# Optimization experiments

Measured on AMD Instinct MI355X. Metric: run time of the kernel, lower is better.

The kernel has to match this reference:

```python
import jax, jax.numpy as jnp
import numpy as np

EMBED_DIM = 128
HIDDEN_DIM = 512
NUM_LAYERS = 2
LATENT_DIM = 128
VOCAB = 2048
BATCH = 4096
NEG = -1.0e9  # matches torch masked fill value -1e9
TEMPERATURE = 1.0  # generate() skips the divide when temperature == 1.0


def _gru_cell(x, h, w_ih, w_hh, b_ih, b_hh):
    # PyTorch GRU cell, gate order (r, z, n)
    gi = x @ w_ih.T + b_ih          # [B, 3H]
    gh = h @ w_hh.T + b_hh          # [B, 3H]
    i_r, i_z, i_n = jnp.split(gi, 3, axis=-1)
    h_r, h_z, h_n = jnp.split(gh, 3, axis=-1)
    r = jax.nn.sigmoid(i_r + h_r)
    u = jax.nn.sigmoid(i_z + h_z)
    n = jnp.tanh(i_n + r * h_n)
    return (1.0 - u) * n + u * h


def setup_inputs() -> dict:
    key = jax.random.key(0)
    ks = jax.random.split(key, 16)

    def unif(k, shape, fan):
        bound = 1.0 / np.sqrt(fan)
        return jax.random.uniform(k, shape, jnp.float32, -bound, bound)

    embed = jax.random.normal(ks[0], (VOCAB, EMBED_DIM), jnp.float32)
    embed = embed.at[0].set(0.0)  # padding_idx = 0

    return dict(
        z=jax.random.normal(ks[1], (BATCH, LATENT_DIM), jnp.float32),
        embed=embed,
        w_lh=unif(ks[2], (NUM_LAYERS * HIDDEN_DIM, LATENT_DIM), LATENT_DIM),
        b_lh=unif(ks[3], (NUM_LAYERS * HIDDEN_DIM,), LATENT_DIM),
        w_ih0=unif(ks[4], (3 * HIDDEN_DIM, EMBED_DIM), HIDDEN_DIM),
        w_hh0=unif(ks[5], (3 * HIDDEN_DIM, HIDDEN_DIM), HIDDEN_DIM),
        b_ih0=unif(ks[6], (3 * HIDDEN_DIM,), HIDDEN_DIM),
        b_hh0=unif(ks[7], (3 * HIDDEN_DIM,), HIDDEN_DIM),
        w_ih1=unif(ks[8], (3 * HIDDEN_DIM, HIDDEN_DIM), HIDDEN_DIM),
        w_hh1=unif(ks[9], (3 * HIDDEN_DIM, HIDDEN_DIM), HIDDEN_DIM),
        b_ih1=unif(ks[10], (3 * HIDDEN_DIM,), HIDDEN_DIM),
        b_hh1=unif(ks[11], (3 * HIDDEN_DIM,), HIDDEN_DIM),
        w_out=unif(ks[12], (VOCAB, HIDDEN_DIM), HIDDEN_DIM),
        b_out=unif(ks[13], (VOCAB,), HIDDEN_DIM),
        bos_idx=1, eos_idx=2, pad_idx=0,
        max_len=64, top_k=40, min_generation_length=20,
    )


def reference(z, embed, w_lh, b_lh, w_ih0, w_hh0, b_ih0, b_hh0,
              w_ih1, w_hh1, b_ih1, b_hh1, w_out, b_out,
              bos_idx, eos_idx, pad_idx, max_len, top_k, min_generation_length):
    B = z.shape[0]
    V = w_out.shape[0]
    H = w_hh0.shape[1]
    eff_min = max(0, min(int(min_generation_length), max(0, max_len - 2)))

    # latent -> initial hidden state [L, B, H]
    h = jnp.tanh(z @ w_lh.T + b_lh).reshape(B, NUM_LAYERS, H).transpose(1, 0, 2)
    rows = jnp.arange(B)[:, None]

    def step(carry, t):
        h, cur, finished, key = carry
        key, sk = jax.random.split(key)
        x = embed[cur]                                   # [B, E]
        h0 = _gru_cell(x, h[0], w_ih0, w_hh0, b_ih0, b_hh0)
        h1 = _gru_cell(h0, h[1], w_ih1, w_hh1, b_ih1, b_hh1)
        logits = h1 @ w_out.T + b_out                    # [B, V]
        logits = logits.at[:, bos_idx].set(NEG).at[:, pad_idx].set(NEG)
        # block EOS until min_generation_length real tokens emitted
        logits = jnp.where((t - 1) < eff_min, logits.at[:, eos_idx].set(NEG), logits)
        if TEMPERATURE != 1.0:
            logits = logits / max(TEMPERATURE, 1e-6)
        if 0 < top_k < V:
            tv, ti = jax.lax.top_k(logits, top_k)
            logits = jnp.full_like(logits, NEG).at[rows, ti].set(tv)
        # multinomial over softmax(logits) == categorical on logits
        nxt = jax.random.categorical(sk, logits).astype(jnp.int32)
        nxt = jnp.where(finished, pad_idx, nxt)
        finished = finished | (nxt == eos_idx)
        return (jnp.stack([h0, h1]), nxt, finished, key), nxt

    init = (h,
            jnp.full((B,), bos_idx, jnp.int32),
            jnp.zeros((B,), dtype=bool),
            jax.random.key(1))
    _, toks = jax.lax.scan(step, init, jnp.arange(1, max_len))  # toks: [max_len-1, B]
    return jnp.concatenate(
        [jnp.full((B, 1), bos_idx, jnp.int32), toks.T.astype(jnp.int32)], axis=1)
```

## Files before the change

kernel.cpp:

```cpp
#include <hip/hip_runtime.h>
#include <cstdint>
#include <cstddef>

#ifndef PARTITIONABLE
#define PARTITIONABLE 1
#endif

namespace {
constexpr int kBatch  = 4096;
constexpr int kEmb    = 128;
constexpr int kHid    = 512;
constexpr int kVoc    = 2048;
constexpr int kMaxLen = 64;
constexpr int kTopK   = 40;
constexpr int kBos = 1, kEos = 2, kPad = 0;
constexpr int kEffMin = 20;
constexpr float kNeg  = -1.0e9f;
constexpr float kTiny = 1.17549435082228751e-38f;
}

typedef __bf16 bf16x8 __attribute__((ext_vector_type(8)));
typedef float  f32x4  __attribute__((ext_vector_type(4)));

__host__ __device__ inline void tf2x32(uint32_t k0, uint32_t k1,
                                       uint32_t x0, uint32_t x1,
                                       uint32_t& o0, uint32_t& o1) {
  uint32_t ks0 = k0, ks1 = k1, ks2 = k0 ^ k1 ^ 0x1BD11BDAu;
  x0 += ks0; x1 += ks1;
#define TFR(r) { x0 += x1; x1 = (x1 << (r)) | (x1 >> (32 - (r))); x1 ^= x0; }
  TFR(13) TFR(15) TFR(26) TFR(6)   x0 += ks1; x1 += ks2 + 1u;
  TFR(17) TFR(29) TFR(16) TFR(24)  x0 += ks2; x1 += ks0 + 2u;
  TFR(13) TFR(15) TFR(26) TFR(6)   x0 += ks0; x1 += ks1 + 3u;
  TFR(17) TFR(29) TFR(16) TFR(24)  x0 += ks1; x1 += ks2 + 4u;
  TFR(13) TFR(15) TFR(26) TFR(6)   x0 += ks2; x1 += ks0 + 5u;
#undef TFR
  o0 = x0; o1 = x1;
}

__device__ __forceinline__ float xla_tanh(float x) {
  float ax = fabsf(x);
  float xc = fminf(fmaxf(x, -9.0f), 9.0f);
  float x2 = __fmul_rn(xc, xc);
  float num = -2.76076847742355e-16f;
  num = __fadd_rn(__fmul_rn(x2, num), 2.00018790482477e-13f);
  num = __fadd_rn(__fmul_rn(x2, num), -8.60467152213735e-11f);
  num = __fadd_rn(__fmul_rn(x2, num), 5.12229709037114e-08f);
  num = __fadd_rn(__fmul_rn(x2, num), 1.48572235717979e-05f);
  num = __fadd_rn(__fmul_rn(x2, num), 6.37261928875436e-04f);
  num = __fadd_rn(__fmul_rn(x2, num), 4.89352455891786e-03f);
  num = __fmul_rn(xc, num);
  float den = 1.19825839466702e-06f;
  den = __fadd_rn(__fmul_rn(x2, den), 1.18534705686654e-04f);
  den = __fadd_rn(__fmul_rn(x2, den), 2.26843463243900e-03f);
  den = __fadd_rn(__fmul_rn(x2, den), 4.89352518554385e-03f);
  return (ax < 4.0e-04f) ? x : __fdiv_rn(num, den);
}

__device__ __forceinline__ float xla_sigmoid(float x) {
  return __fdiv_rn(1.0f, __fadd_rn(1.0f, expf(-x)));
}

__device__ __forceinline__ void gl_lds16(const void* g, void* l) {
  __builtin_amdgcn_global_load_lds(
      (const __attribute__((address_space(1))) void*)g,
      (__attribute__((address_space(3))) void*)l, 16, 0, 0);
}

__device__ __forceinline__ void split3(float a, __bf16& a0, __bf16& a1, __bf16& a2) {
  a0 = (__bf16)a;
  float r1 = __fsub_rn(a, (float)a0);
  a1 = (__bf16)r1;
  float r2 = __fsub_rn(r1, (float)a1);
  a2 = (__bf16)r2;
}

__device__ __forceinline__ float gru_h(float gir, float giz, float gin,
                                       float ghr, float ghz, float ghn,
                                       float hold) {
  float r = xla_sigmoid(__fadd_rn(gir, ghr));
  float u = xla_sigmoid(__fadd_rn(giz, ghz));
  float n = xla_tanh(__fadd_rn(gin, __fmul_rn(r, ghn)));
  float t1 = __fmul_rn(__fsub_rn(1.0f, u), n);
  float t2 = __fmul_rn(u, hold);
  return __fadd_rn(t1, t2);
}

#define MFMA9(c, A0_, A1_, A2_, B0_, B1_, B2_) do {                          \
    c = __builtin_amdgcn_mfma_f32_16x16x32_bf16(A2_, B2_, c, 0, 0, 0);       \
    c = __builtin_amdgcn_mfma_f32_16x16x32_bf16(A2_, B1_, c, 0, 0, 0);       \
    c = __builtin_amdgcn_mfma_f32_16x16x32_bf16(A1_, B2_, c, 0, 0, 0);       \
    c = __builtin_amdgcn_mfma_f32_16x16x32_bf16(A2_, B0_, c, 0, 0, 0);       \
    c = __builtin_amdgcn_mfma_f32_16x16x32_bf16(A1_, B1_, c, 0, 0, 0);       \
    c = __builtin_amdgcn_mfma_f32_16x16x32_bf16(A0_, B2_, c, 0, 0, 0);       \
    c = __builtin_amdgcn_mfma_f32_16x16x32_bf16(A1_, B0_, c, 0, 0, 0);       \
    c = __builtin_amdgcn_mfma_f32_16x16x32_bf16(A0_, B1_, c, 0, 0, 0);       \
    c = __builtin_amdgcn_mfma_f32_16x16x32_bf16(A0_, B0_, c, 0, 0, 0);       \
  } while (0)

template <int ACT>
__global__ __launch_bounds__(256) void gemm2(
    const float* __restrict__ A0, const float* __restrict__ B0,
    const float* __restrict__ bias0, float* __restrict__ C0,
    const float* __restrict__ A1, const float* __restrict__ B1,
    const float* __restrict__ bias1, float* __restrict__ C1,
    int lda, int ldb, int ldc, int K) {
  __shared__ __attribute__((aligned(16))) float As[2][128 * 16];
  __shared__ __attribute__((aligned(16))) float Bs[2][16 * 128];

  const float* A    = blockIdx.z ? A1 : A0;
  const float* Bt   = blockIdx.z ? B1 : B0;
  const float* bias = blockIdx.z ? bias1 : bias0;
  float*       C    = blockIdx.z ? C1 : C0;

  const int tid = threadIdx.x;
  const int w = tid >> 6, l = tid & 63;
  const int bm = blockIdx.y * 128;
  const int bn = blockIdx.x * 128;
  const int tx = tid & 15, ty = tid >> 4;
  const int t3 = ty & 3;

  const int arow  = w * 16 + (l >> 2);
  const int agran = (l & 3) ^ ((l >> 2) & 3);
  const float* pA = A + (size_t)(bm + arow) * lda + agran * 4;
  const int bk = w * 2 + (l >> 5);
  const int bnc = (l & 31) * 4;
  const float* pB = Bt + (size_t)bk * ldb + bn + bnc;

  float acc[8][8];
#pragma unroll
  for (int i = 0; i < 8; ++i)
#pragma unroll
    for (int j = 0; j < 8; ++j) acc[i][j] = 0.0f;

  const int nt = K >> 4;
  gl_lds16(pA,            &As[0][w * 256]);
  gl_lds16(pA + 64 * lda, &As[0][(4 + w) * 256]);
  gl_lds16(pB,            &Bs[0][w * 256]);
  gl_lds16(pB + (size_t)8 * ldb, &Bs[0][(4 + w) * 256]);
  __syncthreads();

  for (int t = 0; t < nt; ++t) {
    const int cur = t & 1;
    if (t + 1 < nt) {
      const float* qA = pA + (t + 1) * 16;
      const float* qB = pB + (size_t)(t + 1) * 16 * ldb;
      gl_lds16(qA,            &As[cur ^ 1][w * 256]);
      gl_lds16(qA + 64 * lda, &As[cur ^ 1][(4 + w) * 256]);
      gl_lds16(qB,            &Bs[cur ^ 1][w * 256]);
      gl_lds16(qB + (size_t)8 * ldb, &Bs[cur ^ 1][(4 + w) * 256]);
    }
    const float* as = As[cur];
    const float* bs = Bs[cur];
#pragma unroll
    for (int g = 0; g < 4; ++g) {
      float4 bv0[4], bv1[4];
#pragma unroll
      for (int q = 0; q < 4; ++q) {
        bv0[q] = *(const float4*)&bs[(g * 4 + q) * 128 + tx * 4];
        bv1[q] = *(const float4*)&bs[(g * 4 + q) * 128 + 64 + tx * 4];
      }
#pragma unroll
      for (int ii = 0; ii < 8; ++ii) {
        float4 a = *(const float4*)&as[(ty + 16 * ii) * 16 + ((g ^ t3) * 4)];
        float ak[4] = {a.x, a.y, a.z, a.w};
#pragma unroll
        for (int q = 0; q < 4; ++q) {
          const float av_ = ak[q];
          const float4 b0 = bv0[q], b1 = bv1[q];
          acc[ii][0] += av_ * b0.x; acc[ii][1] += av_ * b0.y;
          acc[ii][2] += av_ * b0.z; acc[ii][3] += av_ * b0.w;
          acc[ii][4] += av_ * b1.x; acc[ii][5] += av_ * b1.y;
          acc[ii][6] += av_ * b1.z; acc[ii][7] += av_ * b1.w;
        }
      }
    }
    __syncthreads();
  }

  const int c0 = bn + tx * 4, c1 = bn + 64 + tx * 4;
  const float4 bs0 = *(const float4*)&bias[c0];
  const float4 bs1 = *(const float4*)&bias[c1];
#pragma unroll
  for (int ii = 0; ii < 8; ++ii) {
    const int r = bm + ty + 16 * ii;
    float4 o0, o1;
    o0.x = acc[ii][0] + bs0.x; o0.y = acc[ii][1] + bs0.y;
    o0.z = acc[ii][2] + bs0.z; o0.w = acc[ii][3] + bs0.w;
    o1.x = acc[ii][4] + bs1.x; o1.y = acc[ii][5] + bs1.y;
    o1.z = acc[ii][6] + bs1.z; o1.w = acc[ii][7] + bs1.w;
    if (ACT == 1) {
      o0.x = xla_tanh(o0.x); o0.y = xla_tanh(o0.y);
      o0.z = xla_tanh(o0.z); o0.w = xla_tanh(o0.w);
      o1.x = xla_tanh(o1.x); o1.y = xla_tanh(o1.y);
      o1.z = xla_tanh(o1.z); o1.w = xla_tanh(o1.w);
    }
    *(float4*)(C + (size_t)r * ldc + c0) = o0;
    *(float4*)(C + (size_t)r * ldc + c1) = o1;
  }
}

struct GemmArgs {
  const __bf16 *a0, *a1, *a2;
  const __bf16 *b0, *b1, *b2;
  const float* bias;
  float* c;
};

__global__ __launch_bounds__(256, 3) void gemm_mx3(
    GemmArgs g0, GemmArgs g1, int N) {
  __shared__ __attribute__((aligned(16))) __bf16 lds[6 * 4096];

  const GemmArgs g = blockIdx.z ? g1 : g0;
  const int tid = threadIdx.x;
  const int nwg = gridDim.x * gridDim.y;
  const int lin = blockIdx.y * gridDim.x + blockIdx.x;
  const int swz = (lin & 7) * (nwg >> 3) + (lin >> 3);
  const int bm = (swz / gridDim.x) * 128;
  const int bn = (swz % gridDim.x) * 128;
  const int lane = tid & 63;
  const int w  = tid >> 6;
  const int wm = w & 1;
  const int wn = w >> 1;
  const int l15 = lane & 15;
  const int kge = (lane >> 4) * 8;

  const int srow = tid >> 2;
  const int sge  = (tid & 3) * 8;
  const __bf16* tp[6];
  tp[0] = g.a0 + (size_t)(bm + srow) * 512 + sge;
  tp[1] = g.a1 + (size_t)(bm + srow) * 512 + sge;
  tp[2] = g.a2 + (size_t)(bm + srow) * 512 + sge;
  tp[3] = g.b0 + (size_t)(bn + srow) * 512 + sge;
  tp[4] = g.b1 + (size_t)(bn + srow) * 512 + sge;
  tp[5] = g.b2 + (size_t)(bn + srow) * 512 + sge;

  int aoff[4], boff[4];
#pragma unroll
  for (int i = 0; i < 4; ++i) {
    aoff[i] = (wm * 64 + i * 16 + l15) * 32 + kge;
    boff[i] = (wn * 64 + i * 16 + l15) * 32 + kge;
  }

  f32x4 acc[4][4] = {};

  for (int s = 0; s < 16; ++s) {
    const int k0 = s * 32;
#pragma unroll
    for (int p = 0; p < 6; ++p) {
      gl_lds16(tp[p] + k0,                    &lds[p * 4096 + w * 512]);
      gl_lds16(tp[p] + (size_t)64 * 512 + k0, &lds[p * 4096 + 2048 + w * 512]);
    }
    __syncthreads();

    bf16x8 Af[3][4];
#pragma unroll
    for (int mi = 0; mi < 4; ++mi) {
      Af[0][mi] = *(const bf16x8*)&lds[0 * 4096 + aoff[mi]];
      Af[1][mi] = *(const bf16x8*)&lds[1 * 4096 + aoff[mi]];
      Af[2][mi] = *(const bf16x8*)&lds[2 * 4096 + aoff[mi]];
    }
#pragma unroll
    for (int nj = 0; nj < 4; ++nj) {
      bf16x8 B0 = *(const bf16x8*)&lds[3 * 4096 + boff[nj]];
      bf16x8 B1 = *(const bf16x8*)&lds[4 * 4096 + boff[nj]];
      bf16x8 B2 = *(const bf16x8*)&lds[5 * 4096 + boff[nj]];
#pragma unroll
      for (int mi = 0; mi < 4; ++mi) {
        f32x4 c = acc[mi][nj];
        MFMA9(c, Af[0][mi], Af[1][mi], Af[2][mi], B0, B1, B2);
        acc[mi][nj] = c;
      }
    }
    __syncthreads();
  }

#pragma unroll
  for (int mi = 0; mi < 4; ++mi) {
    const int row0 = bm + wm * 64 + mi * 16 + (lane >> 4) * 4;
#pragma unroll
    for (int nj = 0; nj < 4; ++nj) {
      const int col = bn + wn * 64 + nj * 16 + l15;
      const float bv = g.bias[col];
      f32x4 v = acc[mi][nj];
#pragma unroll
      for (int r = 0; r < 4; ++r)
        g.c[(size_t)(row0 + r) * N + col] = v[r] + bv;
    }
  }
}

__global__ __launch_bounds__(256, 2) void gemm_gru0(
    const __bf16* __restrict__ a0, const __bf16* __restrict__ a1,
    const __bf16* __restrict__ a2,
    const __bf16* __restrict__ wb0, const __bf16* __restrict__ wb1,
    const __bf16* __restrict__ wb2,
    const float* __restrict__ bias, const float* __restrict__ Eih0,
    const int* __restrict__ curTok,
    __bf16* __restrict__ q0, __bf16* __restrict__ q1,
    __bf16* __restrict__ q2) {
  __shared__ __attribute__((aligned(16))) __bf16 As[3][4096];
  __shared__ __attribute__((aligned(16))) __bf16 Bs[9][1024];

  const int tid = threadIdx.x;
  const int nwg = gridDim.x * gridDim.y;
  const int lin = blockIdx.y * gridDim.x + blockIdx.x;
  const int swz = (lin & 7) * (nwg >> 3) + (lin >> 3);
  const int bm = (swz / gridDim.x) * 128;
  const int bn = (swz % gridDim.x) * 32;
  const int lane = tid & 63;
  const int w  = tid >> 6;
  const int wm = w & 1;
  const int wn = w >> 1;
  const int l15 = lane & 15;
  const int kge = (lane >> 4) * 8;

  const int srow = tid >> 2;
  const int sge  = (tid & 3) * 8;
  const __bf16* tpA[3];
  tpA[0] = a0 + (size_t)(bm + srow) * 512 + sge;
  tpA[1] = a1 + (size_t)(bm + srow) * 512 + sge;
  tpA[2] = a2 + (size_t)(bm + srow) * 512 + sge;

  const int bcol = lane >> 2;
  const int bge  = (lane & 3) * 8;

  int aoff[4];
#pragma unroll
  for (int i = 0; i < 4; ++i)
    aoff[i] = (wm * 64 + i * 16 + l15) * 32 + kge;
  const int boff = (wn * 16 + l15) * 32 + kge;

  f32x4 acc[3][4] = {};

  for (int s = 0; s < 16; ++s) {
    const int k0 = s * 32;
#pragma unroll
    for (int p = 0; p < 3; ++p) {
      gl_lds16(tpA[p] + k0,                    &As[p][w * 512]);
      gl_lds16(tpA[p] + (size_t)64 * 512 + k0, &As[p][2048 + w * 512]);
    }
    for (int qq = w; qq < 9; qq += 4) {
      const int gg = qq / 3, pp = qq - gg * 3;
      const __bf16* wp = (pp == 0) ? wb0 : (pp == 1) ? wb1 : wb2;
      const __bf16* src =
          wp + (size_t)(gg * 512 + bn + bcol) * 512 + bge + k0;
      gl_lds16(src,                     &Bs[qq][0]);
      gl_lds16(src + (size_t)16 * 512,  &Bs[qq][512]);
    }
    __syncthreads();

    bf16x8 Af[3][4];
#pragma unroll
    for (int mi = 0; mi < 4; ++mi) {
      Af[0][mi] = *(const bf16x8*)&As[0][aoff[mi]];
      Af[1][mi] = *(const bf16x8*)&As[1][aoff[mi]];
      Af[2][mi] = *(const bf16x8*)&As[2][aoff[mi]];
    }
#pragma unroll
    for (int gg = 0; gg < 3; ++gg) {
      bf16x8 B0 = *(const bf16x8*)&Bs[gg * 3 + 0][boff];
      bf16x8 B1 = *(const bf16x8*)&Bs[gg * 3 + 1][boff];
      bf16x8 B2 = *(const bf16x8*)&Bs[gg * 3 + 2][boff];
#pragma unroll
      for (int mi = 0; mi < 4; ++mi) {
        f32x4 c = acc[gg][mi];
        MFMA9(c, Af[0][mi], Af[1][mi], Af[2][mi], B0, B1, B2);
        acc[gg][mi] = c;
      }
    }
    __syncthreads();
  }

  const int col = bn + wn * 16 + l15;
  const float bvr = bias[col];
  const float bvz = bias[512 + col];
  const float bvn = bias[1024 + col];
#pragma unroll
  for (int mi = 0; mi < 4; ++mi) {
    const int row0 = bm + wm * 64 + mi * 16 + (lane >> 4) * 4;
#pragma unroll
    for (int rr = 0; rr < 4; ++rr) {
      const int row = row0 + rr;
      const int tok = curTok[row];
      const float* e = Eih0 + (size_t)tok * 1536;
      const size_t idx = (size_t)row * 512 + col;
      float hold = __fadd_rn(__fadd_rn((float)a0[idx], (float)a1[idx]),
                             (float)a2[idx]);
      float hnew = gru_h(e[col], e[512 + col], e[1024 + col],
                         acc[0][mi][rr] + bvr, acc[1][mi][rr] + bvz,
                         acc[2][mi][rr] + bvn, hold);
      __bf16 s0, s1, s2;
      split3(hnew, s0, s1, s2);
      q0[idx] = s0; q1[idx] = s1; q2[idx] = s2;
    }
  }
}

__global__ __launch_bounds__(256, 2) void gemm_gru1(
    const __bf16* __restrict__ x0, const __bf16* __restrict__ x1,
    const __bf16* __restrict__ x2,
    const __bf16* __restrict__ wi0, const __bf16* __restrict__ wi1,
    const __bf16* __restrict__ wi2,
    const __bf16* __restrict__ wh0, const __bf16* __restrict__ wh1,
    const __bf16* __restrict__ wh2,
    const float* __restrict__ bias_i, const float* __restrict__ bias_h,
    const __bf16* __restrict__ hi0, const __bf16* __restrict__ hi1,
    const __bf16* __restrict__ hi2,
    __bf16* __restrict__ ho0, __bf16* __restrict__ ho1,
    __bf16* __restrict__ ho2) {
  __shared__ __attribute__((aligned(16))) __bf16 As[6][2048];
  __shared__ __attribute__((aligned(16))) __bf16 Bs[18][1024];

  const int tid = threadIdx.x;
  const int nwg = gridDim.x * gridDim.y;
  const int lin = blockIdx.y * gridDim.x + blockIdx.x;
  const int swz = (lin & 7) * (nwg >> 3) + (lin >> 3);
  const int bm = (swz / gridDim.x) * 64;
  const int bn = (swz % gridDim.x) * 32;
  const int lane = tid & 63;
  const int w  = tid >> 6;
  const int wm = w & 1;
  const int wn = w >> 1;
  const int l15 = lane & 15;
  const int kge = (lane >> 4) * 8;

  const int srow = tid >> 2;
  const int sge  = (tid & 3) * 8;
  const __bf16* tpA[6];
  tpA[0] = x0 + (size_t)(bm + srow) * 512 + sge;
  tpA[1] = x1 + (size_t)(bm + srow) * 512 + sge;
  tpA[2] = x2 + (size_t)(bm + srow) * 512 + sge;
  tpA[3] = hi0 + (size_t)(bm + srow) * 512 + sge;
  tpA[4] = hi1 + (size_t)(bm + srow) * 512 + sge;
  tpA[5] = hi2 + (size_t)(bm + srow) * 512 + sge;

  const int bcol = lane >> 2;
  const int bge  = (lane & 3) * 8;

  int aoff[2];
#pragma unroll
  for (int i = 0; i < 2; ++i)
    aoff[i] = (wm * 32 + i * 16 + l15) * 32 + kge;
  const int boff = (wn * 16 + l15) * 32 + kge;

  f32x4 acci[3][2] = {};
  f32x4 acch[3][2] = {};

  const __bf16* wis[3] = {wi0, wi1, wi2};
  const __bf16* whs[3] = {wh0, wh1, wh2};

  for (int s = 0; s < 16; ++s) {
    const int k0 = s * 32;
#pragma unroll
    for (int p = 0; p < 6; ++p)
      gl_lds16(tpA[p] + k0, &As[p][w * 512]);
    for (int qq = w; qq < 18; qq += 4) {
      const int wset = qq / 9;
      const int gg = (qq - wset * 9) / 3, pp = qq - wset * 9 - gg * 3;
      const __bf16* wp = wset ? whs[pp] : wis[pp];
      const __bf16* src = wp + (size_t)(gg * 512 + bn + bcol) * 512 + bge + k0;
      gl_lds16(src,                    &Bs[qq][0]);
      gl_lds16(src + (size_t)16 * 512, &Bs[qq][512]);
    }
    __syncthreads();

    bf16x8 Xf[3][2], Hf[3][2];
#pragma unroll
    for (int mi = 0; mi < 2; ++mi) {
      Xf[0][mi] = *(const bf16x8*)&As[0][aoff[mi]];
      Xf[1][mi] = *(const bf16x8*)&As[1][aoff[mi]];
      Xf[2][mi] = *(const bf16x8*)&As[2][aoff[mi]];
      Hf[0][mi] = *(const bf16x8*)&As[3][aoff[mi]];
      Hf[1][mi] = *(const bf16x8*)&As[4][aoff[mi]];
      Hf[2][mi] = *(const bf16x8*)&As[5][aoff[mi]];
    }
#pragma unroll
    for (int gg = 0; gg < 3; ++gg) {
      bf16x8 Bi0 = *(const bf16x8*)&Bs[gg * 3 + 0][boff];
      bf16x8 Bi1 = *(const bf16x8*)&Bs[gg * 3 + 1][boff];
      bf16x8 Bi2 = *(const bf16x8*)&Bs[gg * 3 + 2][boff];
      bf16x8 Bh0 = *(const bf16x8*)&Bs[9 + gg * 3 + 0][boff];
      bf16x8 Bh1 = *(const bf16x8*)&Bs[9 + gg * 3 + 1][boff];
      bf16x8 Bh2 = *(const bf16x8*)&Bs[9 + gg * 3 + 2][boff];
#pragma unroll
      for (int mi = 0; mi < 2; ++mi) {
        f32x4 ci = acci[gg][mi];
        MFMA9(ci, Xf[0][mi], Xf[1][mi], Xf[2][mi], Bi0, Bi1, Bi2);
        acci[gg][mi] = ci;
        f32x4 ch = acch[gg][mi];
        MFMA9(ch, Hf[0][mi], Hf[1][mi], Hf[2][mi], Bh0, Bh1, Bh2);
        acch[gg][mi] = ch;
      }
    }
    __syncthreads();
  }

  const int col = bn + wn * 16 + l15;
  const float bir = bias_i[col];
  const float biz = bias_i[512 + col];
  const float bin = bias_i[1024 + col];
  const float bhr = bias_h[col];
  const float bhz = bias_h[512 + col];
  const float bhn = bias_h[1024 + col];
#pragma unroll
  for (int mi = 0; mi < 2; ++mi) {
    const int row0 = bm + wm * 32 + mi * 16 + (lane >> 4) * 4;
#pragma unroll
    for (int rr = 0; rr < 4; ++rr) {
      const int row = row0 + rr;
      const size_t idx = (size_t)row * 512 + col;
      float hold = __fadd_rn(__fadd_rn((float)hi0[idx], (float)hi1[idx]),
                             (float)hi2[idx]);
      float hnew = gru_h(acci[0][mi][rr] + bir, acci[1][mi][rr] + biz,
                         acci[2][mi][rr] + bin,
                         acch[0][mi][rr] + bhr, acch[1][mi][rr] + bhz,
                         acch[2][mi][rr] + bhn, hold);
      __bf16 s0, s1, s2;
      split3(hnew, s0, s1, s2);
      ho0[idx] = s0; ho1[idx] = s1; ho2[idx] = s2;
    }
  }
}

__global__ __launch_bounds__(256) void k_split(
    const float* __restrict__ in, __bf16* __restrict__ p0,
    __bf16* __restrict__ p1, __bf16* __restrict__ p2, int total) {
  int i = blockIdx.x * 256 + threadIdx.x;
  if (i >= total) return;
  __bf16 a0, a1, a2;
  split3(in[i], a0, a1, a2);
  p0[i] = a0; p1[i] = a1; p2[i] = a2;
}

__global__ __launch_bounds__(256) void k_transpose(
    const float* __restrict__ in, float* __restrict__ out, int R, int C) {
  __shared__ float tile[32][33];
  int c0 = blockIdx.x * 32, r0 = blockIdx.y * 32;
  int x = threadIdx.x, y0 = threadIdx.y;
  for (int i = y0; i < 32; i += 8) {
    int r = r0 + i, c = c0 + x;
    tile[i][x] = (r < R && c < C) ? in[(size_t)r * C + c] : 0.0f;
  }
  __syncthreads();
  for (int i = y0; i < 32; i += 8) {
    int orow = c0 + i, oc = r0 + x;
    if (orow < C && oc < R) out[(size_t)orow * R + oc] = tile[x][i];
  }
}

__global__ __launch_bounds__(256) void k_sample(
    const float* __restrict__ logits, int* __restrict__ cur,
    int* __restrict__ finished, int* __restrict__ outTok,
    int t, uint32_t sk0, uint32_t sk1) {
  const int row = blockIdx.x;
  const int tid = threadIdx.x;
  __shared__ float sl[kVoc];
  __shared__ uint32_t skeys[kVoc];
  __shared__ int   redi[4];
  __shared__ float redf[4];
  __shared__ int   redix[4];

  const float* lp = logits + (size_t)row * kVoc;
  for (int c = tid; c < kVoc; c += 256) {
    float v = lp[c];
    if (c == kBos || c == kPad) v = kNeg;
    if (c == kEos && t < 1 + kEffMin) v = kNeg;
    sl[c] = v;
    uint32_t u = __float_as_uint(v);
    skeys[c] = u ^ ((u >> 31) ? 0xFFFFFFFFu : 0x80000000u);
  }
  __syncthreads();

  uint32_t prefix = 0u;
  for (int b = 31; b >= 0; --b) {
    uint32_t trial = prefix | (1u << b);
    int cnt = 0;
    for (int c = tid; c < kVoc; c += 256) cnt += (skeys[c] >= trial) ? 1 : 0;
#pragma unroll
    for (int off = 32; off; off >>= 1) cnt += __shfl_down(cnt, off, 64);
    __syncthreads();
    if ((tid & 63) == 0) redi[tid >> 6] = cnt;
    __syncthreads();
    int total = redi[0] + redi[1] + redi[2] + redi[3];
    if (total >= kTopK) prefix = trial;
  }

  float best = -3.4e38f; int bidx = kVoc;
  for (int c = tid; c < kVoc; c += 256) {
    if (skeys[c] >= prefix) {
      uint32_t idx = (uint32_t)row * (uint32_t)kVoc + (uint32_t)c;
      uint32_t w1, w2, bits;
#if PARTITIONABLE
      tf2x32(sk0, sk1, 0u, idx, w1, w2);
      bits = w1 ^ w2;
#else
      const uint32_t HH = (uint32_t)((uint64_t)kBatch * kVoc / 2);
      if (idx < HH) { tf2x32(sk0, sk1, idx, idx + HH, w1, w2); bits = w1; }
      else          { tf2x32(sk0, sk1, idx - HH, idx, w1, w2); bits = w2; }
#endif
      uint32_t fb = (bits >> 9) | 0x3f800000u;
      float uf = __fsub_rn(__uint_as_float(fb), 1.0f);
      if (uf == 0.0f) uf = kTiny;
      float g = -logf(-logf(uf));
      float tot = __fadd_rn(g, sl[c]);
      if (tot > best || (tot == best && c < bidx)) { best = tot; bidx = c; }
    }
  }
#pragma unroll
  for (int off = 32; off; off >>= 1) {
    float ov = __shfl_down(best, off, 64);
    int   oi = __shfl_down(bidx, off, 64);
    if (ov > best || (ov == best && oi < bidx)) { best = ov; bidx = oi; }
  }
  if ((tid & 63) == 0) { redf[tid >> 6] = best; redix[tid >> 6] = bidx; }
  __syncthreads();
  if (tid == 0) {
    for (int w = 1; w < 4; ++w) {
      if (redf[w] > best || (redf[w] == best && redix[w] < bidx)) {
        best = redf[w]; bidx = redix[w];
      }
    }
    int fin = finished[row];
    int nxt = fin ? kPad : bidx;
    outTok[(size_t)row * kMaxLen + t] = nxt;
    cur[row] = nxt;
    finished[row] = fin | (nxt == kEos);
  }
}

__global__ __launch_bounds__(256) void k_init(int* cur, int* finished, int* outTok) {
  int i = blockIdx.x * 256 + threadIdx.x;
  if (i < kBatch) {
    cur[i] = kBos;
    finished[i] = 0;
    outTok[(size_t)i * kMaxLen] = kBos;
  }
}

extern "C" void kernel_launch(void* const* d_in, const int* in_sizes, int n_in,
                              void* d_out, int out_size, void* d_ws, size_t ws_size,
                              hipStream_t stream) {
  (void)in_sizes; (void)n_in; (void)out_size; (void)ws_size;
  const float* z      = (const float*)d_in[0];
  const float* embed  = (const float*)d_in[1];
  const float* w_lh   = (const float*)d_in[2];
  const float* b_lh   = (const float*)d_in[3];
  const float* w_ih0  = (const float*)d_in[4];
  const float* w_hh0  = (const float*)d_in[5];
  const float* b_ih0  = (const float*)d_in[6];
  const float* b_hh0  = (const float*)d_in[7];
  const float* w_ih1  = (const float*)d_in[8];
  const float* w_hh1  = (const float*)d_in[9];
  const float* b_ih1  = (const float*)d_in[10];
  const float* b_hh1  = (const float*)d_in[11];
  const float* w_out  = (const float*)d_in[12];
  const float* b_out  = (const float*)d_in[13];
  int* out = (int*)d_out;

  char* base = (char*)d_ws;
  int* curTok   = (int*)base;
  int* finished = curTok + kBatch;
  __bf16* q = (__bf16*)(base + 32768);
  __bf16* whh0[3]; __bf16* wih1[3]; __bf16* whh1[3]; __bf16* wout[3];
  for (int i = 0; i < 3; ++i) { whh0[i] = q; q += (size_t)1536 * 512; }
  for (int i = 0; i < 3; ++i) { wih1[i] = q; q += (size_t)1536 * 512; }
  for (int i = 0; i < 3; ++i) { whh1[i] = q; q += (size_t)1536 * 512; }
  for (int i = 0; i < 3; ++i) { wout[i] = q; q += (size_t)2048 * 512; }
  __bf16* hs0A[3]; __bf16* hs1A[3];
  for (int i = 0; i < 3; ++i) { hs0A[i] = q; q += (size_t)kBatch * kHid; }
  for (int i = 0; i < 3; ++i) { hs1A[i] = q; q += (size_t)kBatch * kHid; }
  float* f = (float*)q;
  float* Eih0 = f; f += (size_t)kVoc * 1536;
  float* ghA  = f; f += (size_t)kBatch * 1536;
  float* gi1  = f; f += (size_t)kBatch * 1536;
  float* logits = ghA;
  float* wt_ih0 = ghA;
  float* wt_lh  = ghA + (size_t)128 * 1536;
  float* h0tmp  = gi1;
  float* h1tmp  = gi1 + (size_t)kBatch * kHid;
  __bf16* hs0B[3];
  { __bf16* hb = (__bf16*)f;
    for (int i = 0; i < 3; ++i) { hs0B[i] = hb; hb += (size_t)kBatch * kHid; } }
  __bf16* hs1B[3];
  {
    __bf16* hb = (__bf16*)(gi1 + (size_t)kBatch * kHid);
    for (int i = 0; i < 3; ++i) { hs1B[i] = hb; hb += (size_t)kBatch * kHid; } }

  dim3 blk(256);
  dim3 tblk(32, 8);

  k_transpose<<<dim3(4, 48), tblk, 0, stream>>>(w_ih0, wt_ih0, 1536, 128);
  k_transpose<<<dim3(4, 32), tblk, 0, stream>>>(w_lh,  wt_lh,  1024, 128);
  k_split<<<dim3(1536 * 512 / 256), blk, 0, stream>>>(w_hh0, whh0[0], whh0[1], whh0[2], 1536 * 512);
  k_split<<<dim3(1536 * 512 / 256), blk, 0, stream>>>(w_ih1, wih1[0], wih1[1], wih1[2], 1536 * 512);
  k_split<<<dim3(1536 * 512 / 256), blk, 0, stream>>>(w_hh1, whh1[0], whh1[1], whh1[2], 1536 * 512);
  k_split<<<dim3(2048 * 512 / 256), blk, 0, stream>>>(w_out, wout[0], wout[1], wout[2], 2048 * 512);

  gemm2<0><<<dim3(12, 16, 1), blk, 0, stream>>>(
      embed, wt_ih0, b_ih0, Eih0, embed, wt_ih0, b_ih0, Eih0,
      kEmb, 1536, 1536, kEmb);
  gemm2<1><<<dim3(4, 32, 2), blk, 0, stream>>>(
      z, wt_lh,       b_lh,       h0tmp,
      z, wt_lh + 512, b_lh + 512, h1tmp,
      kEmb, 1024, kHid, kEmb);
  k_split<<<dim3(kBatch * kHid / 256), blk, 0, stream>>>(h0tmp, hs0A[0], hs0A[1], hs0A[2], kBatch * kHid);
  k_split<<<dim3(kBatch * kHid / 256), blk, 0, stream>>>(h1tmp, hs1A[0], hs1A[1], hs1A[2], kBatch * kHid);
  k_init<<<dim3((kBatch + 255) / 256), blk, 0, stream>>>(curTok, finished, out);

  uint32_t key0 = 0u, key1 = 1u;
  for (int t = 1; t < kMaxLen; ++t) {
    uint32_t nk0, nk1, s0, s1;
#if PARTITIONABLE
    tf2x32(key0, key1, 0u, 0u, nk0, nk1);
    tf2x32(key0, key1, 0u, 1u, s0, s1);
#else
    uint32_t a0, b0w, a1, b1w;
    tf2x32(key0, key1, 0u, 2u, a0, b0w);
    tf2x32(key0, key1, 1u, 3u, a1, b1w);
    nk0 = a0; nk1 = a1; s0 = b0w; s1 = b1w;
#endif
    __bf16** h0in  = (t & 1) ? hs0A : hs0B;
    __bf16** h0out = (t & 1) ? hs0B : hs0A;
    __bf16** h1in  = (t & 1) ? hs1A : hs1B;
    __bf16** h1out = (t & 1) ? hs1B : hs1A;

    gemm_gru0<<<dim3(16, 32), blk, 0, stream>>>(
        h0in[0], h0in[1], h0in[2], whh0[0], whh0[1], whh0[2],
        b_hh0, Eih0, curTok, h0out[0], h0out[1], h0out[2]);

    gemm_gru1<<<dim3(16, 64), blk, 0, stream>>>(
        h0out[0], h0out[1], h0out[2],
        wih1[0], wih1[1], wih1[2],
        whh1[0], whh1[1], whh1[2],
        b_ih1, b_hh1,
        h1in[0], h1in[1], h1in[2],
        h1out[0], h1out[1], h1out[2]);

    GemmArgs gla{h1out[0], h1out[1], h1out[2], wout[0], wout[1], wout[2], b_out, logits};
    gemm_mx3<<<dim3(16, 32, 1), blk, 0, stream>>>(gla, gla, 2048);
    k_sample<<<dim3(kBatch), blk, 0, stream>>>(logits, curTok, finished, out, t, s0, s1);

    key0 = nk0; key1 = nk1;
  }
}
```

Measured before the change: 19.81 ms.

## Enlarge GRU1 M-tile with phased X/H loads; radix-select top-k threshold

The layer-1 GRU GEMM now uses a 128-row M tile and half as many blocks. It processes the input and hidden products in two phases per K step that share one set of LDS buffers, so each weight tile is reused across more rows. The sampler's 32-iteration bitwise threshold search is replaced by a 4-pass byte radix histogram with suffix scan, which cuts the number of sweeps and barriers over the vocabulary. In exchange, each K step has more barriers, fewer workgroups are resident, and accumulator registers per thread double, which may hurt occupancy.

```diff
diff --git a/kernel.cpp b/kernel.cpp
--- a/kernel.cpp
+++ b/kernel.cpp
@@ -408,14 +408,14 @@
     const __bf16* __restrict__ hi2,
     __bf16* __restrict__ ho0, __bf16* __restrict__ ho1,
     __bf16* __restrict__ ho2) {
-  __shared__ __attribute__((aligned(16))) __bf16 As[6][2048];
-  __shared__ __attribute__((aligned(16))) __bf16 Bs[18][1024];
+  __shared__ __attribute__((aligned(16))) __bf16 As[3][4096];
+  __shared__ __attribute__((aligned(16))) __bf16 Bs[9][1024];
 
   const int tid = threadIdx.x;
   const int nwg = gridDim.x * gridDim.y;
   const int lin = blockIdx.y * gridDim.x + blockIdx.x;
   const int swz = (lin & 7) * (nwg >> 3) + (lin >> 3);
-  const int bm = (swz / gridDim.x) * 64;
+  const int bm = (swz / gridDim.x) * 128;
   const int bn = (swz % gridDim.x) * 32;
   const int lane = tid & 63;
   const int w  = tid >> 6;
@@ -426,70 +426,96 @@
 
   const int srow = tid >> 2;
   const int sge  = (tid & 3) * 8;
-  const __bf16* tpA[6];
-  tpA[0] = x0 + (size_t)(bm + srow) * 512 + sge;
-  tpA[1] = x1 + (size_t)(bm + srow) * 512 + sge;
-  tpA[2] = x2 + (size_t)(bm + srow) * 512 + sge;
-  tpA[3] = hi0 + (size_t)(bm + srow) * 512 + sge;
-  tpA[4] = hi1 + (size_t)(bm + srow) * 512 + sge;
-  tpA[5] = hi2 + (size_t)(bm + srow) * 512 + sge;
+  const __bf16* tpX[3];
+  tpX[0] = x0 + (size_t)(bm + srow) * 512 + sge;
+  tpX[1] = x1 + (size_t)(bm + srow) * 512 + sge;
+  tpX[2] = x2 + (size_t)(bm + srow) * 512 + sge;
+  const __bf16* tpH[3];
+  tpH[0] = hi0 + (size_t)(bm + srow) * 512 + sge;
+  tpH[1] = hi1 + (size_t)(bm + srow) * 512 + sge;
+  tpH[2] = hi2 + (size_t)(bm + srow) * 512 + sge;
 
   const int bcol = lane >> 2;
   const int bge  = (lane & 3) * 8;
 
-  int aoff[2];
-#pragma unroll
-  for (int i = 0; i < 2; ++i)
-    aoff[i] = (wm * 32 + i * 16 + l15) * 32 + kge;
+  int aoff[4];
+#pragma unroll
+  for (int i = 0; i < 4; ++i)
+    aoff[i] = (wm * 64 + i * 16 + l15) * 32 + kge;
   const int boff = (wn * 16 + l15) * 32 + kge;
 
-  f32x4 acci[3][2] = {};
-  f32x4 acch[3][2] = {};
-
-  const __bf16* wis[3] = {wi0, wi1, wi2};
-  const __bf16* whs[3] = {wh0, wh1, wh2};
+  f32x4 acci[3][4] = {};
+  f32x4 acch[3][4] = {};
 
   for (int s = 0; s < 16; ++s) {
     const int k0 = s * 32;
 #pragma unroll
-    for (int p = 0; p < 6; ++p)
-      gl_lds16(tpA[p] + k0, &As[p][w * 512]);
-    for (int qq = w; qq < 18; qq += 4) {
-      const int wset = qq / 9;
-      const int gg = (qq - wset * 9) / 3, pp = qq - wset * 9 - gg * 3;
-      const __bf16* wp = wset ? whs[pp] : wis[pp];
+    for (int p = 0; p < 3; ++p) {
+      gl_lds16(tpX[p] + k0,                    &As[p][w * 512]);
+      gl_lds16(tpX[p] + (size_t)64 * 512 + k0, &As[p][2048 + w * 512]);
+    }
+    for (int qq = w; qq < 9; qq += 4) {
+      const int gg = qq / 3, pp = qq - gg * 3;
+      const __bf16* wp = (pp == 0) ? wi0 : (pp == 1) ? wi1 : wi2;
       const __bf16* src = wp + (size_t)(gg * 512 + bn + bcol) * 512 + bge + k0;
       gl_lds16(src,                    &Bs[qq][0]);
       gl_lds16(src + (size_t)16 * 512, &Bs[qq][512]);
     }
     __syncthreads();
-
-    bf16x8 Xf[3][2], Hf[3][2];
-#pragma unroll
-    for (int mi = 0; mi < 2; ++mi) {
-      Xf[0][mi] = *(const bf16x8*)&As[0][aoff[mi]];
-      Xf[1][mi] = *(const bf16x8*)&As[1][aoff[mi]];
-      Xf[2][mi] = *(const bf16x8*)&As[2][aoff[mi]];
-      Hf[0][mi] = *(const bf16x8*)&As[3][aoff[mi]];
-      Hf[1][mi] = *(const bf16x8*)&As[4][aoff[mi]];
-      Hf[2][mi] = *(const bf16x8*)&As[5][aoff[mi]];
-    }
-#pragma unroll
-    for (int gg = 0; gg < 3; ++gg) {
-      bf16x8 Bi0 = *(const bf16x8*)&Bs[gg * 3 + 0][boff];
-      bf16x8 Bi1 = *(const bf16x8*)&Bs[gg * 3 + 1][boff];
-      bf16x8 Bi2 = *(const bf16x8*)&Bs[gg * 3 + 2][boff];
-      bf16x8 Bh0 = *(const bf16x8*)&Bs[9 + gg * 3 + 0][boff];
-      bf16x8 Bh1 = *(const bf16x8*)&Bs[9 + gg * 3 + 1][boff];
-      bf16x8 Bh2 = *(const bf16x8*)&Bs[9 + gg * 3 + 2][boff];
-#pragma unroll
-      for (int mi = 0; mi < 2; ++mi) {
-        f32x4 ci = acci[gg][mi];
-        MFMA9(ci, Xf[0][mi], Xf[1][mi], Xf[2][mi], Bi0, Bi1, Bi2);
-        acci[gg][mi] = ci;
-        f32x4 ch = acch[gg][mi];
-        MFMA9(ch, Hf[0][mi], Hf[1][mi], Hf[2][mi], Bh0, Bh1, Bh2);
-        acch[gg][mi] = ch;
+    {
+      bf16x8 Af[3][4];
+#pragma unroll
+      for (int mi = 0; mi < 4; ++mi) {
+        Af[0][mi] = *(const bf16x8*)&As[0][aoff[mi]];
+        Af[1][mi] = *(const bf16x8*)&As[1][aoff[mi]];
+        Af[2][mi] = *(const bf16x8*)&As[2][aoff[mi]];
+      }
+#pragma unroll
+      for (int gg = 0; gg < 3; ++gg) {
+        bf16x8 B0 = *(const bf16x8*)&Bs[gg * 3 + 0][boff];
+        bf16x8 B1 = *(const bf16x8*)&Bs[gg * 3 + 1][boff];
+        bf16x8 B2 = *(const bf16x8*)&Bs[gg * 3 + 2][boff];
+#pragma unroll
+        for (int mi = 0; mi < 4; ++mi) {
+          f32x4 c = acci[gg][mi];
+          MFMA9(c, Af[0][mi], Af[1][mi], Af[2][mi], B0, B1, B2);
+          acci[gg][mi] = c;
+        }
+      }
+    }
+    __syncthreads();
+#pragma unroll
+    for (int p = 0; p < 3; ++p) {
+      gl_lds16(tpH[p] + k0,                    &As[p][w * 512]);
+      gl_lds16(tpH[p] + (size_t)64 * 512 + k0, &As[p][2048 + w * 512]);
+    }
+    for (int qq = w; qq < 9; qq += 4) {
+      const int gg = qq / 3, pp = qq - gg * 3;
+      const __bf16* wp = (pp == 0) ? wh0 : (pp == 1) ? wh1 : wh2;
+      const __bf16* src = wp + (size_t)(gg * 512 + bn + bcol) * 512 + bge + k0;
+      gl_lds16(src,                    &Bs[qq][0]);
+      gl_lds16(src + (size_t)16 * 512, &Bs[qq][512]);
+    }
+    __syncthreads();
+    {
+      bf16x8 Hf[3][4];
+#pragma unroll
+      for (int mi = 0; mi < 4; ++mi) {
+        Hf[0][mi] = *(const bf16x8*)&As[0][aoff[mi]];
+        Hf[1][mi] = *(const bf16x8*)&As[1][aoff[mi]];
+        Hf[2][mi] = *(const bf16x8*)&As[2][aoff[mi]];
+      }
+#pragma unroll
+      for (int gg = 0; gg < 3; ++gg) {
+        bf16x8 B0 = *(const bf16x8*)&Bs[gg * 3 + 0][boff];
+        bf16x8 B1 = *(const bf16x8*)&Bs[gg * 3 + 1][boff];
+        bf16x8 B2 = *(const bf16x8*)&Bs[gg * 3 + 2][boff];
+#pragma unroll
+        for (int mi = 0; mi < 4; ++mi) {
+          f32x4 c = acch[gg][mi];
+          MFMA9(c, Hf[0][mi], Hf[1][mi], Hf[2][mi], B0, B1, B2);
+          acch[gg][mi] = c;
+        }
       }
     }
     __syncthreads();
@@ -503,8 +529,8 @@
   const float bhz = bias_h[512 + col];
   const float bhn = bias_h[1024 + col];
 #pragma unroll
-  for (int mi = 0; mi < 2; ++mi) {
-    const int row0 = bm + wm * 32 + mi * 16 + (lane >> 4) * 4;
+  for (int mi = 0; mi < 4; ++mi) {
+    const int row0 = bm + wm * 64 + mi * 16 + (lane >> 4) * 4;
 #pragma unroll
     for (int rr = 0; rr < 4; ++rr) {
       const int row = row0 + rr;
@@ -556,7 +582,11 @@
   const int tid = threadIdx.x;
   __shared__ float sl[kVoc];
   __shared__ uint32_t skeys[kVoc];
-  __shared__ int   redi[4];
+  __shared__ int  cnt[256];
+  __shared__ int  sfx[257];
+  __shared__ int  wtot[4];
+  __shared__ uint32_t sPrefix;
+  __shared__ int  sNeed;
   __shared__ float redf[4];
   __shared__ int   redix[4];
 
@@ -572,17 +602,40 @@
   __syncthreads();
 
   uint32_t prefix = 0u;
-  for (int b = 31; b >= 0; --b) {
-    uint32_t trial = prefix | (1u << b);
-    int cnt = 0;
-    for (int c = tid; c < kVoc; c += 256) cnt += (skeys[c] >= trial) ? 1 : 0;
-#pragma unroll
-    for (int off = 32; off; off >>= 1) cnt += __shfl_down(cnt, off, 64);
-    __syncthreads();
-    if ((tid & 63) == 0) redi[tid >> 6] = cnt;
-    __syncthreads();
-    int total = redi[0] + redi[1] + redi[2] + redi[3];
-    if (total >= kTopK) prefix = trial;
+  int need = kTopK;
+  const int lane = tid & 63, wv = tid >> 6;
+  for (int by = 3; by >= 0; --by) {
+    cnt[tid] = 0;
+    __syncthreads();
+    const int sh = by * 8;
+    const uint32_t hiMask = (by == 3) ? 0u : (0xFFFFFFFFu << (sh + 8));
+    for (int c = tid; c < kVoc; c += 256) {
+      uint32_t k = skeys[c];
+      if ((k & hiMask) == prefix) atomicAdd(&cnt[(k >> sh) & 255], 1);
+    }
+    __syncthreads();
+    int val = cnt[tid];
+#pragma unroll
+    for (int off = 1; off < 64; off <<= 1) {
+      int other = __shfl_down(val, off, 64);
+      if (lane + off < 64) val += other;
+    }
+    int wt = __shfl(val, 0, 64);
+    if (lane == 0) wtot[wv] = wt;
+    __syncthreads();
+    int tail = 0;
+    for (int u = wv + 1; u < 4; ++u) tail += wtot[u];
+    sfx[tid] = val + tail;
+    if (tid == 0) sfx[256] = 0;
+    __syncthreads();
+    if (sfx[tid] >= need && sfx[tid + 1] < need) {
+      sPrefix = prefix | ((uint32_t)tid << sh);
+      sNeed = need - sfx[tid + 1];
+    }
+    __syncthreads();
+    prefix = sPrefix;
+    need = sNeed;
+    __syncthreads();
   }
 
   float best = -3.4e38f; int bidx = kVoc;
@@ -728,7 +781,7 @@
         h0in[0], h0in[1], h0in[2], whh0[0], whh0[1], whh0[2],
         b_hh0, Eih0, curTok, h0out[0], h0out[1], h0out[2]);
 
-    gemm_gru1<<<dim3(16, 64), blk, 0, stream>>>(
+    gemm_gru1<<<dim3(16, 32), blk, 0, stream>>>(
         h0out[0], h0out[1], h0out[2],
         wih1[0], wih1[1], wih1[2],
         whh1[0], whh1[1], whh1[2],
```

Measured after the change: 15.89 ms. 1.25x faster.
